# Kernel tuning notes

Measured on AMD Instinct MI355X. Metric: run time of the kernel, lower is better.

The kernel has to match this reference:

```python
import jax, jax.numpy as jnp
import numpy as np

EMBED_DIM = 1024
N_HEADS = 16

def setup_inputs() -> dict:
    key = jax.random.key(0)
    ks = jax.random.split(key, 5)
    C = EMBED_DIM
    std = 1.0 / np.sqrt(C)
    x = jax.random.normal(ks[0], (2, 2048, C), dtype=jnp.float32)
    w_attn = jax.random.normal(ks[1], (C, 3 * C), dtype=jnp.float32) * std  # (in, out)
    b_attn = jax.random.normal(ks[2], (3 * C,), dtype=jnp.float32) * 0.01
    w_proj = jax.random.normal(ks[3], (C, C), dtype=jnp.float32) * std
    b_proj = jax.random.normal(ks[4], (C,), dtype=jnp.float32) * 0.01
    return {"x": x, "w_attn": w_attn, "b_attn": b_attn, "w_proj": w_proj, "b_proj": b_proj}

def reference(x, w_attn, b_attn, w_proj, b_proj):
    B, T, C = x.shape
    H = N_HEADS
    D = C // H
    qkv = x @ w_attn + b_attn                      # (B, T, 3C)
    q, k, v = jnp.split(qkv, 3, axis=2)
    # (B, T, C) -> (B, H, T, D)
    q = q.reshape(B, T, H, D).transpose(0, 2, 1, 3)
    k = k.reshape(B, T, H, D).transpose(0, 2, 1, 3)
    v = v.reshape(B, T, H, D).transpose(0, 2, 1, 3)
    # Faithful to source: query is divided by scale BEFORE QK^T, and the
    # similarity is divided by scale AGAIN before softmax (net scale = 1/D).
    scale = jnp.asarray(D, dtype=x.dtype) ** 0.5
    q = q / scale
    sim = jnp.einsum('bhnd,bhsd->bhns', q, k)      # (B, H, T, T)
    causal = jnp.tril(jnp.ones((T, T), dtype=bool))
    neg_min = jnp.finfo(sim.dtype).min
    sim = jnp.where(causal[None, None, :, :], sim, neg_min)
    attn = jax.nn.softmax(sim / scale, axis=-1)
    out = jnp.einsum('bhns,bhsd->bhnd', attn, v)   # (B, H, T, D)
    # source: gqa returns (b n h d), forward does transpose(1,2) -> (b h n d)
    # then .view(B, T, C); net effect is reshaping the (B,H,T,D) layout.
    y = out.reshape(B, T, C)
    y = y @ w_proj + b_proj
    return y
```

## Files before the change

kernel.cpp:

```cpp
#include <hip/hip_runtime.h>
#include <hip/hip_bf16.h>

#define BB 2
#define TT 2048
#define CC 1024
#define HH 16
#define DD 64
#define MM (BB*TT)
#define QSZ ((size_t)MM*CC)

#define QSCALE 0.022542110013890053f

typedef __attribute__((ext_vector_type(8))) short bf16x8;
typedef __attribute__((ext_vector_type(4))) float f32x4;
typedef __attribute__((address_space(1))) const unsigned char as1_u8;
typedef __attribute__((address_space(3))) unsigned char as3_u8;

struct alignas(8) bf16x4_s { __hip_bfloat16 h[4]; };

__constant__ unsigned char U_qi[48] = {
    15,31,30,31, 14,29,30,28,29, 13,27,28,26,27, 12,25,26,24,25,
    11,23,24,22,23, 10,21,22,20,21, 9,19,20,18,19, 8,17,18,16,17,
    7,16, 6,5,4,3,2,1,0};
__constant__ unsigned char U_t0[48] = {
    0,0,15,16, 0,0,0,14,15, 0,0,0,13,14, 0,0,0,12,13,
    0,0,0,11,12, 0,0,0,10,11, 0,0,0,9,10, 0,0,0,8,9,
    0,0, 0,0,0,0,0,0,0};
__constant__ unsigned char U_t1[48] = {
    16,16,31,32, 15,15,15,29,30, 14,14,14,27,28, 13,13,13,25,26,
    12,12,12,23,24, 11,11,11,21,22, 10,10,10,19,20, 9,9,9,17,18,
    8,8, 7,6,5,4,3,2,1};

__global__ __launch_bounds__(256) void convert_bf16(
    const float* __restrict__ in, __hip_bfloat16* __restrict__ outp, int n)
{
    const int i = (blockIdx.x * 256 + threadIdx.x) * 8;
    if (i + 8 <= n) {
        const float4 a = *(const float4*)&in[i];
        const float4 b = *(const float4*)&in[i + 4];
        __hip_bfloat16 tmp[8];
        tmp[0] = __float2bfloat16(a.x); tmp[1] = __float2bfloat16(a.y);
        tmp[2] = __float2bfloat16(a.z); tmp[3] = __float2bfloat16(a.w);
        tmp[4] = __float2bfloat16(b.x); tmp[5] = __float2bfloat16(b.y);
        tmp[6] = __float2bfloat16(b.z); tmp[7] = __float2bfloat16(b.w);
        *(float4*)&outp[i] = *(float4*)&tmp[0];
    }
}

__global__ __launch_bounds__(256) void transpose_convert(
    const float* __restrict__ in, __hip_bfloat16* __restrict__ outp, int R, int Cc)
{
    __shared__ float tile[64][68];
    const int c0 = blockIdx.x * 64, r0 = blockIdx.y * 64;
    const int t = threadIdx.x;
    {
        const int r = t >> 2, cb = (t & 3) * 16;
        #pragma unroll
        for (int i = 0; i < 4; ++i)
            *(float4*)&tile[r][cb + i*4] = *(const float4*)&in[(size_t)(r0 + r)*Cc + c0 + cb + i*4];
    }
    __syncthreads();
    {
        const int c = t >> 2, rb = (t & 3) * 16;
        __hip_bfloat16 tmp[16];
        #pragma unroll
        for (int j = 0; j < 16; ++j) tmp[j] = __float2bfloat16(tile[rb + j][c]);
        __hip_bfloat16* dst = outp + (size_t)(c0 + c)*R + r0 + rb;
        *(float4*)&dst[0] = *(float4*)&tmp[0];
        *(float4*)&dst[8] = *(float4*)&tmp[8];
    }
}

template<int MODE>
__global__ __launch_bounds__(256) void gemm_mfma(
    const __hip_bfloat16* __restrict__ A,
    const __hip_bfloat16* __restrict__ BT,
    const float* __restrict__ bias,
    void* __restrict__ out, int M, int N, int K)
{
    __shared__ __hip_bfloat16 As[128][64];
    __shared__ __hip_bfloat16 Bs[128][64];

    const int tid = threadIdx.x;
    const int w = tid >> 6, l = tid & 63;
    const int lr = l & 15, lg = l >> 4;
    const int wr = w >> 1, wc = w & 1;
    const int rsw = (lr & 7) << 4;
    const int lsw = ((l & 7) ^ (l >> 3)) * 8;

    const int nwg = gridDim.x * gridDim.y;
    const int bid = blockIdx.y * gridDim.x + blockIdx.x;
    const int swz_id = (bid & 7) * (nwg >> 3) + (bid >> 3);
    const int row0 = (swz_id / gridDim.x) * 128;
    const int col0 = (swz_id % gridDim.x) * 128;

    f32x4 acc[4][4] = {};

    for (int k0 = 0; k0 < K; k0 += 64) {
        __syncthreads();
        #pragma unroll
        for (int i = 0; i < 4; ++i) {
            const int br = w*32 + i*8;
            const __hip_bfloat16* ga = A  + (size_t)(row0 + br + (l>>3))*K + k0 + lsw;
            __builtin_amdgcn_global_load_lds((as1_u8*)ga, (as3_u8*)&As[br][0], 16, 0, 0);
            const __hip_bfloat16* gb = BT + (size_t)(col0 + br + (l>>3))*K + k0 + lsw;
            __builtin_amdgcn_global_load_lds((as1_u8*)gb, (as3_u8*)&Bs[br][0], 16, 0, 0);
        }
        __syncthreads();

        #pragma unroll
        for (int s = 0; s < 2; ++s) {
            bf16x8 af[4], bfr[4];
            #pragma unroll
            for (int m = 0; m < 4; ++m) {
                const char* ab = (const char*)&As[wr*64 + m*16 + lr][0];
                af[m] = *(const bf16x8*)(ab + ((s*64 + lg*16) ^ rsw));
            }
            #pragma unroll
            for (int n = 0; n < 4; ++n) {
                const char* bb = (const char*)&Bs[wc*64 + n*16 + lr][0];
                bfr[n] = *(const bf16x8*)(bb + ((s*64 + lg*16) ^ rsw));
            }
            #pragma unroll
            for (int m = 0; m < 4; ++m)
                #pragma unroll
                for (int n = 0; n < 4; ++n)
                    acc[m][n] = __builtin_amdgcn_mfma_f32_16x16x32_bf16(af[m], bfr[n], acc[m][n], 0, 0, 0);
        }
    }

    #pragma unroll
    for (int m = 0; m < 4; ++m) {
        #pragma unroll
        for (int n = 0; n < 4; ++n) {
            const int ng = col0 + wc*64 + n*16 + lr;
            const float bv = bias[ng];
            const int mg0 = row0 + wr*64 + m*16 + lg*4;
            if (MODE == 0) {
                const int which = ng >> 10, c = ng & 1023;
                const int h = c >> 6, d = c & 63;
                if (which == 2) {
                    const int b = mg0 >> 11, t0 = mg0 & 2047;
                    bf16x4_s pk;
                    #pragma unroll
                    for (int r = 0; r < 4; ++r)
                        pk.h[r] = __float2bfloat16(acc[m][n][r] + bv);
                    *(bf16x4_s*)((__hip_bfloat16*)out + (size_t)2*QSZ +
                        (((size_t)(b*HH + h))*DD + d)*TT + t0) = pk;
                } else {
                    #pragma unroll
                    for (int r = 0; r < 4; ++r) {
                        const int mg = mg0 + r;
                        float v = acc[m][n][r] + bv;
                        if (which == 0) v *= QSCALE;
                        const int b = mg >> 11, t = mg & 2047;
                        ((__hip_bfloat16*)out)[(size_t)which*QSZ +
                            (((size_t)(b*HH + h))*TT + t)*DD + d] = __float2bfloat16(v);
                    }
                }
            } else {
                #pragma unroll
                for (int r = 0; r < 4; ++r)
                    ((float*)out)[(size_t)(mg0 + r)*N + ng] = acc[m][n][r] + bv;
            }
        }
    }
}

__global__ __launch_bounds__(256) void attn_mfma(
    const __hip_bfloat16* __restrict__ Qb,
    const __hip_bfloat16* __restrict__ Kb,
    const __hip_bfloat16* __restrict__ Vb,
    __hip_bfloat16* __restrict__ Ob,
    __hip_bfloat16* __restrict__ Opart,
    float* __restrict__ Lpart)
{
    __shared__ __hip_bfloat16 k_lds[64][64];
    __shared__ __hip_bfloat16 vT[64][64];
    __shared__ __hip_bfloat16 p_lds[4][16][64];

    const int tid = threadIdx.x;
    const int w  = tid >> 6;
    const int l  = tid & 63;
    const int lr = l & 15;
    const int lg = l >> 4;
    const int swz = (lr & 7) << 4;

    const int bid = blockIdx.x;
    const int sid = (bid & 7) * 192 + (bid >> 3);
    const int bh  = sid / 48;
    const int u   = sid % 48;
    const int qi  = U_qi[u];
    const int t0i = U_t0[u];
    const int t1i = U_t1[u];
    const int qb  = qi * 64;

    const __hip_bfloat16* Qh = Qb + (size_t)bh*TT*DD;
    const __hip_bfloat16* Kh = Kb + (size_t)bh*TT*DD;
    const __hip_bfloat16* Vh = Vb + (size_t)bh*DD*TT;

    bf16x8 qa[2];
    const int qrow = qb + w*16 + lr;
    {
        const __hip_bfloat16* qp = Qh + (size_t)qrow*DD + lg*8;
        qa[0] = *(const bf16x8*)(qp);
        qa[1] = *(const bf16x8*)(qp + 32);
    }

    const int srow = tid >> 2, sch = tid & 3;
    const int wswz = (srow & 7) << 4;

    float4 kr0, kr1, vr0, vr1;
    {
        const __hip_bfloat16* ksrc = Kh + (size_t)(t0i*64 + srow)*DD + sch*16;
        const __hip_bfloat16* vsrc = Vh + (size_t)srow*TT + t0i*64 + sch*16;
        kr0 = *(const float4*)ksrc; kr1 = *(const float4*)(ksrc + 8);
        vr0 = *(const float4*)vsrc; vr1 = *(const float4*)(vsrc + 8);
    }
    {
        char* krow = (char*)&k_lds[srow][0];
        char* vrow = (char*)&vT[srow][0];
        *(float4*)(krow + ((sch*32)      ^ wswz)) = kr0;
        *(float4*)(krow + ((sch*32 + 16) ^ wswz)) = kr1;
        *(float4*)(vrow + ((sch*32)      ^ wswz)) = vr0;
        *(float4*)(vrow + ((sch*32 + 16) ^ wswz)) = vr1;
    }
    __syncthreads();

    f32x4 oacc[4] = {};
    float l_r = 0.f;

    for (int t = t0i; t < t1i; ++t) {
        const int kv0 = t * 64;
        const bool has_next = (t + 1 < t1i);

        if (has_next) {
            const int kv1 = kv0 + 64;
            const __hip_bfloat16* ksrc = Kh + (size_t)(kv1 + srow)*DD + sch*16;
            const __hip_bfloat16* vsrc = Vh + (size_t)srow*TT + kv1 + sch*16;
            kr0 = *(const float4*)ksrc; kr1 = *(const float4*)(ksrc + 8);
            vr0 = *(const float4*)vsrc; vr1 = *(const float4*)(vsrc + 8);
        }

        f32x4 sacc[4] = {};
        #pragma unroll
        for (int mt = 0; mt < 4; ++mt) {
            const char* kbase = (const char*)&k_lds[mt*16 + lr][0];
            const bf16x8 kb0 = *(const bf16x8*)(kbase + ((     16*lg) ^ swz));
            const bf16x8 kb1 = *(const bf16x8*)(kbase + ((64 + 16*lg) ^ swz));
            sacc[mt] = __builtin_amdgcn_mfma_f32_16x16x32_bf16(kb0, qa[0], sacc[mt], 0, 0, 0);
            sacc[mt] = __builtin_amdgcn_mfma_f32_16x16x32_bf16(kb1, qa[1], sacc[mt], 0, 0, 0);
        }

        if (t == qi) {
            #pragma unroll
            for (int mt = 0; mt < 4; ++mt)
                #pragma unroll
                for (int r = 0; r < 4; ++r)
                    if (kv0 + mt*16 + lg*4 + r > qrow) sacc[mt][r] = -3.0e38f;
        }
        __hip_bfloat16* prow = &p_lds[w][lr][0];
        #pragma unroll
        for (int mt = 0; mt < 4; ++mt) {
            bf16x4_s pk;
            #pragma unroll
            for (int r = 0; r < 4; ++r) {
                const float p = exp2f(sacc[mt][r]);
                l_r += p;
                pk.h[r] = __float2bfloat16(p);
            }
            *(bf16x4_s*)((char*)prow + ((32*mt + 8*lg) ^ swz)) = pk;
        }

        const bf16x8 pb0 = *(const bf16x8*)((const char*)prow + ((     16*lg) ^ swz));
        const bf16x8 pb1 = *(const bf16x8*)((const char*)prow + ((64 + 16*lg) ^ swz));
        #pragma unroll
        for (int dt = 0; dt < 4; ++dt) {
            const char* vbase = (const char*)&vT[dt*16 + lr][0];
            const bf16x8 vb0 = *(const bf16x8*)(vbase + ((     16*lg) ^ swz));
            const bf16x8 vb1 = *(const bf16x8*)(vbase + ((64 + 16*lg) ^ swz));
            oacc[dt] = __builtin_amdgcn_mfma_f32_16x16x32_bf16(vb0, pb0, oacc[dt], 0, 0, 0);
            oacc[dt] = __builtin_amdgcn_mfma_f32_16x16x32_bf16(vb1, pb1, oacc[dt], 0, 0, 0);
        }

        if (has_next) {
            __syncthreads();
            char* krow = (char*)&k_lds[srow][0];
            char* vrow = (char*)&vT[srow][0];
            *(float4*)(krow + ((sch*32)      ^ wswz)) = kr0;
            *(float4*)(krow + ((sch*32 + 16) ^ wswz)) = kr1;
            *(float4*)(vrow + ((sch*32)      ^ wswz)) = vr0;
            *(float4*)(vrow + ((sch*32 + 16) ^ wswz)) = vr1;
            __syncthreads();
        }
    }

    l_r += __shfl_xor(l_r, 16);
    l_r += __shfl_xor(l_r, 32);

    if (qi >= 16) {
        const int s = (t0i != 0);
        const int unit = ((bh*16 + (qi - 16)) << 1) | s;
        const int rowu = w*16 + lr;
        __hip_bfloat16* Oprow = Opart + ((size_t)unit*64 + rowu)*64;
        #pragma unroll
        for (int dt = 0; dt < 4; ++dt) {
            bf16x4_s ok;
            #pragma unroll
            for (int r = 0; r < 4; ++r)
                ok.h[r] = __float2bfloat16(oacc[dt][r]);
            *(bf16x4_s*)(Oprow + dt*16 + lg*4) = ok;
        }
        if (lg == 0) Lpart[unit*64 + rowu] = l_r;
    } else {
        __hip_bfloat16* Orow = Ob + ((size_t)bh*TT + qrow)*DD;
        const float inv = 1.0f / l_r;
        #pragma unroll
        for (int dt = 0; dt < 4; ++dt) {
            bf16x4_s ok;
            #pragma unroll
            for (int r = 0; r < 4; ++r)
                ok.h[r] = __float2bfloat16(oacc[dt][r] * inv);
            *(bf16x4_s*)(Orow + dt*16 + lg*4) = ok;
        }
    }
}

__global__ __launch_bounds__(256) void attn_combine(
    const __hip_bfloat16* __restrict__ Opart,
    const float* __restrict__ Lpart,
    __hip_bfloat16* __restrict__ Ob)
{
    const int w = threadIdx.x >> 6, d = threadIdx.x & 63;
    const int rowg = blockIdx.x * 4 + w;
    const int r  = rowg & 63;
    const int jj = (rowg >> 6) & 15;
    const int bh = rowg >> 10;
    const int u0 = (bh*16 + jj) << 1;
    const float inv = 1.0f / (Lpart[u0*64 + r] + Lpart[(u0 + 1)*64 + r]);
    const float o1 = __bfloat162float(Opart[((size_t)u0*64 + r)*64 + d]);
    const float o2 = __bfloat162float(Opart[((size_t)(u0 + 1)*64 + r)*64 + d]);
    const int qrow = (16 + jj)*64 + r;
    Ob[((size_t)bh*TT + qrow)*DD + d] = __float2bfloat16((o1 + o2) * inv);
}

extern "C" void kernel_launch(void* const* d_in, const int* in_sizes, int n_in,
                              void* d_out, int out_size, void* d_ws, size_t ws_size,
                              hipStream_t stream)
{
    const float* x      = (const float*)d_in[0];
    const float* w_attn = (const float*)d_in[1];
    const float* b_attn = (const float*)d_in[2];
    const float* w_proj = (const float*)d_in[3];
    const float* b_proj = (const float*)d_in[4];
    float* out = (float*)d_out;

    __hip_bfloat16* xb     = (__hip_bfloat16*)d_ws;
    __hip_bfloat16* wqkvT  = xb + QSZ;
    __hip_bfloat16* wprojT = wqkvT + 3*CC*CC;
    __hip_bfloat16* Qb     = wprojT + CC*CC;
    __hip_bfloat16* Kb     = Qb + QSZ;
    __hip_bfloat16* Vt     = Kb + QSZ;
    __hip_bfloat16* Ob     = Vt + QSZ;

    __hip_bfloat16* Opart  = xb;
    float*          Lpart  = (float*)wqkvT;

    convert_bf16<<<dim3(QSZ/(256*8)), 256, 0, stream>>>(x, xb, (int)QSZ);
    transpose_convert<<<dim3(3*CC/64, CC/64), 256, 0, stream>>>(w_attn, wqkvT, CC, 3*CC);
    transpose_convert<<<dim3(CC/64, CC/64), 256, 0, stream>>>(w_proj, wprojT, CC, CC);

    gemm_mfma<0><<<dim3(3*CC/128, MM/128), 256, 0, stream>>>(xb, wqkvT, b_attn, (void*)Qb, MM, 3*CC, CC);

    attn_mfma<<<dim3(32*48), 256, 0, stream>>>(Qb, Kb, Vt, Ob, Opart, Lpart);

    attn_combine<<<dim3(32768/4), 256, 0, stream>>>(Opart, Lpart, Ob);

    gemm_mfma<1><<<dim3(CC/128, MM/128), 256, 0, stream>>>(Ob, wprojT, b_proj, (void*)out, MM, CC, CC);
}
```

Measured before the change: 123.4 us.

## Fuse prep kernels, use packed bf16 converts, and tune attention inner loop

Merges the x conversion and the two weight transpose-converts into a single launch dispatched by block index, removing two kernel launches. Replaces scalar float-to-bf16 conversions with packed v_cvt_pk_bf16_f32 inline asm throughout. In the attention kernel it precomputes LDS addresses and offsets, advances global K/V pointers incrementally, splits the row-sum into per-tile accumulators, and raises wave priority around the MFMA blocks. The packed convert may round differently from the library routine, and the setprio hints may or may not help scheduling.

```diff
diff --git a/kernel.cpp b/kernel.cpp
--- a/kernel.cpp
+++ b/kernel.cpp
@@ -17,6 +17,12 @@
 typedef __attribute__((address_space(3))) unsigned char as3_u8;
 
 struct alignas(8) bf16x4_s { __hip_bfloat16 h[4]; };
+
+static __device__ __forceinline__ unsigned cvt_pk_bf16(float lo, float hi) {
+    unsigned r;
+    asm("v_cvt_pk_bf16_f32 %0, %1, %2" : "=v"(r) : "v"(lo), "v"(hi));
+    return r;
+}
 
 __constant__ unsigned char U_qi[48] = {
     15,31,30,31, 14,29,30,28,29, 13,27,28,26,27, 12,25,26,24,25,
@@ -31,28 +37,29 @@
     12,12,12,23,24, 11,11,11,21,22, 10,10,10,19,20, 9,9,9,17,18,
     8,8, 7,6,5,4,3,2,1};
 
-__global__ __launch_bounds__(256) void convert_bf16(
-    const float* __restrict__ in, __hip_bfloat16* __restrict__ outp, int n)
-{
-    const int i = (blockIdx.x * 256 + threadIdx.x) * 8;
-    if (i + 8 <= n) {
-        const float4 a = *(const float4*)&in[i];
-        const float4 b = *(const float4*)&in[i + 4];
-        __hip_bfloat16 tmp[8];
-        tmp[0] = __float2bfloat16(a.x); tmp[1] = __float2bfloat16(a.y);
-        tmp[2] = __float2bfloat16(a.z); tmp[3] = __float2bfloat16(a.w);
-        tmp[4] = __float2bfloat16(b.x); tmp[5] = __float2bfloat16(b.y);
-        tmp[6] = __float2bfloat16(b.z); tmp[7] = __float2bfloat16(b.w);
-        *(float4*)&outp[i] = *(float4*)&tmp[0];
-    }
-}
-
-__global__ __launch_bounds__(256) void transpose_convert(
-    const float* __restrict__ in, __hip_bfloat16* __restrict__ outp, int R, int Cc)
+__global__ __launch_bounds__(256) void prep_kernel(
+    const float* __restrict__ x,  __hip_bfloat16* __restrict__ xb,
+    const float* __restrict__ wa, __hip_bfloat16* __restrict__ wqkvT,
+    const float* __restrict__ wp, __hip_bfloat16* __restrict__ wprojT)
 {
     __shared__ float tile[64][68];
-    const int c0 = blockIdx.x * 64, r0 = blockIdx.y * 64;
     const int t = threadIdx.x;
+    const int b = blockIdx.x;
+    if (b < 2048) {
+        const int i = (b * 256 + t) * 8;
+        const float4 a = *(const float4*)&x[i];
+        const float4 c = *(const float4*)&x[i + 4];
+        uint2 lo, hi;
+        lo.x = cvt_pk_bf16(a.x, a.y); lo.y = cvt_pk_bf16(a.z, a.w);
+        hi.x = cvt_pk_bf16(c.x, c.y); hi.y = cvt_pk_bf16(c.z, c.w);
+        *(uint2*)&xb[i] = lo;
+        *(uint2*)&xb[i + 4] = hi;
+        return;
+    }
+    const float* in; __hip_bfloat16* outp; int R, Cc, bx, by;
+    if (b < 2816) { const int i = b - 2048; in = wa; outp = wqkvT; R = CC; Cc = 3*CC; bx = i % 48; by = i / 48; }
+    else          { const int i = b - 2816; in = wp; outp = wprojT; R = CC; Cc = CC;  bx = i % 16; by = i / 16; }
+    const int c0 = bx * 64, r0 = by * 64;
     {
         const int r = t >> 2, cb = (t & 3) * 16;
         #pragma unroll
@@ -62,12 +69,18 @@
     __syncthreads();
     {
         const int c = t >> 2, rb = (t & 3) * 16;
-        __hip_bfloat16 tmp[16];
-        #pragma unroll
-        for (int j = 0; j < 16; ++j) tmp[j] = __float2bfloat16(tile[rb + j][c]);
+        uint2 o0, o1;
+        o0.x = cvt_pk_bf16(tile[rb+0][c],  tile[rb+1][c]);
+        o0.y = cvt_pk_bf16(tile[rb+2][c],  tile[rb+3][c]);
+        o1.x = cvt_pk_bf16(tile[rb+4][c],  tile[rb+5][c]);
+        o1.y = cvt_pk_bf16(tile[rb+6][c],  tile[rb+7][c]);
         __hip_bfloat16* dst = outp + (size_t)(c0 + c)*R + r0 + rb;
-        *(float4*)&dst[0] = *(float4*)&tmp[0];
-        *(float4*)&dst[8] = *(float4*)&tmp[8];
+        *(uint2*)&dst[0] = o0; *(uint2*)&dst[4] = o1;
+        o0.x = cvt_pk_bf16(tile[rb+8][c],  tile[rb+9][c]);
+        o0.y = cvt_pk_bf16(tile[rb+10][c], tile[rb+11][c]);
+        o1.x = cvt_pk_bf16(tile[rb+12][c], tile[rb+13][c]);
+        o1.y = cvt_pk_bf16(tile[rb+14][c], tile[rb+15][c]);
+        *(uint2*)&dst[8] = o0; *(uint2*)&dst[12] = o1;
     }
 }
 
@@ -141,12 +154,11 @@
                 const int h = c >> 6, d = c & 63;
                 if (which == 2) {
                     const int b = mg0 >> 11, t0 = mg0 & 2047;
-                    bf16x4_s pk;
-                    #pragma unroll
-                    for (int r = 0; r < 4; ++r)
-                        pk.h[r] = __float2bfloat16(acc[m][n][r] + bv);
-                    *(bf16x4_s*)((__hip_bfloat16*)out + (size_t)2*QSZ +
-                        (((size_t)(b*HH + h))*DD + d)*TT + t0) = pk;
+                    uint2 pv;
+                    pv.x = cvt_pk_bf16(acc[m][n][0] + bv, acc[m][n][1] + bv);
+                    pv.y = cvt_pk_bf16(acc[m][n][2] + bv, acc[m][n][3] + bv);
+                    *(uint2*)((__hip_bfloat16*)out + (size_t)2*QSZ +
+                        (((size_t)(b*HH + h))*DD + d)*TT + t0) = pv;
                 } else {
                     #pragma unroll
                     for (int r = 0; r < 4; ++r) {
@@ -207,50 +219,54 @@
         qa[1] = *(const bf16x8*)(qp + 32);
     }
 
+    const int off0 = (16*lg) ^ swz;
+    const int off1 = (64 + 16*lg) ^ swz;
+    const char* kr0b = (const char*)&k_lds[lr][0];
+    const char* vr0b = (const char*)&vT[lr][0];
+    char* pwb = (char*)&p_lds[w][lr][0];
+    int pwo[4];
+    #pragma unroll
+    for (int mt = 0; mt < 4; ++mt) pwo[mt] = (32*mt + 8*lg) ^ swz;
+
     const int srow = tid >> 2, sch = tid & 3;
     const int wswz = (srow & 7) << 4;
-
-    float4 kr0, kr1, vr0, vr1;
-    {
-        const __hip_bfloat16* ksrc = Kh + (size_t)(t0i*64 + srow)*DD + sch*16;
-        const __hip_bfloat16* vsrc = Vh + (size_t)srow*TT + t0i*64 + sch*16;
-        kr0 = *(const float4*)ksrc; kr1 = *(const float4*)(ksrc + 8);
-        vr0 = *(const float4*)vsrc; vr1 = *(const float4*)(vsrc + 8);
-    }
-    {
-        char* krow = (char*)&k_lds[srow][0];
-        char* vrow = (char*)&vT[srow][0];
-        *(float4*)(krow + ((sch*32)      ^ wswz)) = kr0;
-        *(float4*)(krow + ((sch*32 + 16) ^ wswz)) = kr1;
-        *(float4*)(vrow + ((sch*32)      ^ wswz)) = vr0;
-        *(float4*)(vrow + ((sch*32 + 16) ^ wswz)) = vr1;
-    }
+    char* kwr = (char*)&k_lds[srow][0];
+    char* vwr = (char*)&vT[srow][0];
+    const int wo0 = (sch*32) ^ wswz, wo1 = (sch*32 + 16) ^ wswz;
+
+    const __hip_bfloat16* ksrc = Kh + (size_t)(t0i*64 + srow)*DD + sch*16;
+    const __hip_bfloat16* vsrc = Vh + (size_t)srow*TT + t0i*64 + sch*16;
+
+    float4 kr0 = *(const float4*)ksrc, kr1 = *(const float4*)(ksrc + 8);
+    float4 vr0 = *(const float4*)vsrc, vr1 = *(const float4*)(vsrc + 8);
+    ksrc += 64*DD; vsrc += 64;
+    *(float4*)(kwr + wo0) = kr0; *(float4*)(kwr + wo1) = kr1;
+    *(float4*)(vwr + wo0) = vr0; *(float4*)(vwr + wo1) = vr1;
     __syncthreads();
 
     f32x4 oacc[4] = {};
-    float l_r = 0.f;
+    f32x4 lacc = {0.f, 0.f, 0.f, 0.f};
 
     for (int t = t0i; t < t1i; ++t) {
         const int kv0 = t * 64;
         const bool has_next = (t + 1 < t1i);
 
         if (has_next) {
-            const int kv1 = kv0 + 64;
-            const __hip_bfloat16* ksrc = Kh + (size_t)(kv1 + srow)*DD + sch*16;
-            const __hip_bfloat16* vsrc = Vh + (size_t)srow*TT + kv1 + sch*16;
             kr0 = *(const float4*)ksrc; kr1 = *(const float4*)(ksrc + 8);
             vr0 = *(const float4*)vsrc; vr1 = *(const float4*)(vsrc + 8);
+            ksrc += 64*DD; vsrc += 64;
         }
 
         f32x4 sacc[4] = {};
+        __builtin_amdgcn_s_setprio(1);
         #pragma unroll
         for (int mt = 0; mt < 4; ++mt) {
-            const char* kbase = (const char*)&k_lds[mt*16 + lr][0];
-            const bf16x8 kb0 = *(const bf16x8*)(kbase + ((     16*lg) ^ swz));
-            const bf16x8 kb1 = *(const bf16x8*)(kbase + ((64 + 16*lg) ^ swz));
+            const bf16x8 kb0 = *(const bf16x8*)(kr0b + mt*2048 + off0);
+            const bf16x8 kb1 = *(const bf16x8*)(kr0b + mt*2048 + off1);
             sacc[mt] = __builtin_amdgcn_mfma_f32_16x16x32_bf16(kb0, qa[0], sacc[mt], 0, 0, 0);
             sacc[mt] = __builtin_amdgcn_mfma_f32_16x16x32_bf16(kb1, qa[1], sacc[mt], 0, 0, 0);
         }
+        __builtin_amdgcn_s_setprio(0);
 
         if (t == qi) {
             #pragma unroll
@@ -259,42 +275,38 @@
                 for (int r = 0; r < 4; ++r)
                     if (kv0 + mt*16 + lg*4 + r > qrow) sacc[mt][r] = -3.0e38f;
         }
-        __hip_bfloat16* prow = &p_lds[w][lr][0];
         #pragma unroll
         for (int mt = 0; mt < 4; ++mt) {
-            bf16x4_s pk;
-            #pragma unroll
-            for (int r = 0; r < 4; ++r) {
-                const float p = exp2f(sacc[mt][r]);
-                l_r += p;
-                pk.h[r] = __float2bfloat16(p);
-            }
-            *(bf16x4_s*)((char*)prow + ((32*mt + 8*lg) ^ swz)) = pk;
-        }
-
-        const bf16x8 pb0 = *(const bf16x8*)((const char*)prow + ((     16*lg) ^ swz));
-        const bf16x8 pb1 = *(const bf16x8*)((const char*)prow + ((64 + 16*lg) ^ swz));
+            const float p0 = exp2f(sacc[mt][0]), p1 = exp2f(sacc[mt][1]);
+            const float p2 = exp2f(sacc[mt][2]), p3 = exp2f(sacc[mt][3]);
+            lacc[mt] += (p0 + p1) + (p2 + p3);
+            uint2 pp;
+            pp.x = cvt_pk_bf16(p0, p1);
+            pp.y = cvt_pk_bf16(p2, p3);
+            *(uint2*)(pwb + pwo[mt]) = pp;
+        }
+
+        const bf16x8 pb0 = *(const bf16x8*)(pwb + off0);
+        const bf16x8 pb1 = *(const bf16x8*)(pwb + off1);
+        __builtin_amdgcn_s_setprio(1);
         #pragma unroll
         for (int dt = 0; dt < 4; ++dt) {
-            const char* vbase = (const char*)&vT[dt*16 + lr][0];
-            const bf16x8 vb0 = *(const bf16x8*)(vbase + ((     16*lg) ^ swz));
-            const bf16x8 vb1 = *(const bf16x8*)(vbase + ((64 + 16*lg) ^ swz));
+            const bf16x8 vb0 = *(const bf16x8*)(vr0b + dt*2048 + off0);
+            const bf16x8 vb1 = *(const bf16x8*)(vr0b + dt*2048 + off1);
             oacc[dt] = __builtin_amdgcn_mfma_f32_16x16x32_bf16(vb0, pb0, oacc[dt], 0, 0, 0);
             oacc[dt] = __builtin_amdgcn_mfma_f32_16x16x32_bf16(vb1, pb1, oacc[dt], 0, 0, 0);
         }
+        __builtin_amdgcn_s_setprio(0);
 
         if (has_next) {
             __syncthreads();
-            char* krow = (char*)&k_lds[srow][0];
-            char* vrow = (char*)&vT[srow][0];
-            *(float4*)(krow + ((sch*32)      ^ wswz)) = kr0;
-            *(float4*)(krow + ((sch*32 + 16) ^ wswz)) = kr1;
-            *(float4*)(vrow + ((sch*32)      ^ wswz)) = vr0;
-            *(float4*)(vrow + ((sch*32 + 16) ^ wswz)) = vr1;
+            *(float4*)(kwr + wo0) = kr0; *(float4*)(kwr + wo1) = kr1;
+            *(float4*)(vwr + wo0) = vr0; *(float4*)(vwr + wo1) = vr1;
             __syncthreads();
         }
     }
 
+    float l_r = (lacc[0] + lacc[1]) + (lacc[2] + lacc[3]);
     l_r += __shfl_xor(l_r, 16);
     l_r += __shfl_xor(l_r, 32);
 
@@ -305,11 +317,10 @@
         __hip_bfloat16* Oprow = Opart + ((size_t)unit*64 + rowu)*64;
         #pragma unroll
         for (int dt = 0; dt < 4; ++dt) {
-            bf16x4_s ok;
-            #pragma unroll
-            for (int r = 0; r < 4; ++r)
-                ok.h[r] = __float2bfloat16(oacc[dt][r]);
-            *(bf16x4_s*)(Oprow + dt*16 + lg*4) = ok;
+            uint2 ov;
+            ov.x = cvt_pk_bf16(oacc[dt][0], oacc[dt][1]);
+            ov.y = cvt_pk_bf16(oacc[dt][2], oacc[dt][3]);
+            *(uint2*)(Oprow + dt*16 + lg*4) = ov;
         }
         if (lg == 0) Lpart[unit*64 + rowu] = l_r;
     } else {
@@ -317,11 +328,10 @@
         const float inv = 1.0f / l_r;
         #pragma unroll
         for (int dt = 0; dt < 4; ++dt) {
-            bf16x4_s ok;
-            #pragma unroll
-            for (int r = 0; r < 4; ++r)
-                ok.h[r] = __float2bfloat16(oacc[dt][r] * inv);
-            *(bf16x4_s*)(Orow + dt*16 + lg*4) = ok;
+            uint2 ov;
+            ov.x = cvt_pk_bf16(oacc[dt][0]*inv, oacc[dt][1]*inv);
+            ov.y = cvt_pk_bf16(oacc[dt][2]*inv, oacc[dt][3]*inv);
+            *(uint2*)(Orow + dt*16 + lg*4) = ov;
         }
     }
 }
@@ -366,9 +376,7 @@
     __hip_bfloat16* Opart  = xb;
     float*          Lpart  = (float*)wqkvT;
 
-    convert_bf16<<<dim3(QSZ/(256*8)), 256, 0, stream>>>(x, xb, (int)QSZ);
-    transpose_convert<<<dim3(3*CC/64, CC/64), 256, 0, stream>>>(w_attn, wqkvT, CC, 3*CC);
-    transpose_convert<<<dim3(CC/64, CC/64), 256, 0, stream>>>(w_proj, wprojT, CC, CC);
+    prep_kernel<<<dim3(3072), 256, 0, stream>>>(x, xb, w_attn, wqkvT, w_proj, wprojT);
 
     gemm_mfma<0><<<dim3(3*CC/128, MM/128), 256, 0, stream>>>(xb, wqkvT, b_attn, (void*)Qb, MM, 3*CC, CC);
 
```

Result: faster. 115.2 us (-6.7%).
